# Kernel optimization log

Hardware: AMD Instinct MI355X
Metric: run time of the kernel (lower is better)

## Reference

```python
import jax, jax.numpy as jnp
import numpy as np

B, CIN, COUT, K, L = 32, 128, 128, 7, 4096
STRIDE, PAD = 1, 3
TEMP = 1.0


def setup_inputs() -> dict:
    key = jax.random.key(0)
    k1, k2 = jax.random.split(key)
    x = jax.random.normal(k1, (B, CIN, L), dtype=jnp.float32)
    weight = jax.random.normal(k2, (COUT, CIN, K), dtype=jnp.float32) * 0.1  # init: normal(0, 0.1)
    bias = jnp.zeros((COUT,), dtype=jnp.float32)
    return {"x": x, "weight": weight, "bias": bias}


def reference(x, weight, bias):
    # Soft tropical conv (intended math of the module):
    #   y[b,o,w] = T * logsumexp_{c,k}( (x[b,c,w*stride+k] + W[o,c,k]) / T ) + bias[o]
    # with -inf padding (exp(-inf)=0 => plain zero padding in exp space).
    # Computed as a numerically-stabilized standard conv in exp space, which is
    # mathematically identical and avoids materializing the (B,O,C,K,L) tensor.
    xm = jnp.max(x)
    wm = jnp.max(weight)
    ex = jnp.exp((x - xm) / TEMP)          # (B, CIN, L)
    ew = jnp.exp((weight - wm) / TEMP)     # (COUT, CIN, K)
    s = jax.lax.conv_general_dilated(
        ex, ew,
        window_strides=(STRIDE,),
        padding=[(PAD, PAD)],
        dimension_numbers=("NCH", "OIH", "NCH"),
    )  # (B, COUT, L_out); cross-correlation, matching torch unfold indexing x[i+k]
    y = TEMP * jnp.log(s) + (xm + wm)
    return y + bias[None, :, None]
```

## Files before the change

### kernel.cpp

```cpp
#include <hip/hip_runtime.h>
#include <hip/hip_bf16.h>
#include <cstdint>
#include <cstddef>

#define B_N   32
#define CIN_  128
#define COUT_ 128
#define KW_   7
#define L_    4096
#define PAD_  3
#define NW_   256
#define BC_   32
#define RPB   4104
#define NWELEM (KW_ * COUT_ * CIN_)
#define NGUARD (B_N * 8 * CIN_)

#define SW_ELEMS (KW_ * COUT_ * BC_)
#define SX_ROWS  320
#define SX_ELEMS (SX_ROWS * BC_)
#define NGRAN_W  (SW_ELEMS / 8)
#define NGRAN_T  ((SW_ELEMS + SX_ELEMS) / 8)

typedef __attribute__((ext_vector_type(8))) short  bf16x8;
typedef __attribute__((ext_vector_type(4))) float  f32x4;

__device__ __forceinline__ void gl2lds16(const void* g, void* l) {
    __builtin_amdgcn_global_load_lds(
        (const __attribute__((address_space(1))) unsigned int*)g,
        (__attribute__((address_space(3))) unsigned int*)l, 16, 0, 0);
}

__global__ __launch_bounds__(256) void exp_x_kernel(
        const float* __restrict__ x, __hip_bfloat16* __restrict__ exT,
        const float* __restrict__ w, __hip_bfloat16* __restrict__ ewb) {
    if (blockIdx.x >= 64) {
        if (blockIdx.y != 0) return;
        int base = (blockIdx.x - 64) * 256 + threadIdx.x;
        #pragma unroll
        for (int i = 0; i < 32; ++i) {
            int idx = base + 4608 * i;
            if (idx < NWELEM) {
                int c = idx & 127, rest = idx >> 7;
                int o = rest & 127, k = rest >> 7;
                ewb[idx] = __float2bfloat16(__expf(w[(o * CIN_ + c) * KW_ + k]));
            } else {
                int j  = idx - NWELEM;
                int b  = j >> 10, rr = (j >> 7) & 7, c = j & 127;
                int r  = (rr < 3) ? rr : (4096 + rr);
                exT[((size_t)b * RPB + r) * CIN_ + c] = __float2bfloat16(0.0f);
            }
        }
        return;
    }

    __shared__ __align__(16) __hip_bfloat16 tileT[64 * 136];
    const int b  = blockIdx.y;
    const int l0 = blockIdx.x * 64;
    const int tid = threadIdx.x;
    const float* xb = x + (size_t)b * CIN_ * L_ + l0;

    #pragma unroll
    for (int i = 0; i < 8; ++i) {
        int idx = tid + 256 * i;
        int c   = idx >> 4;
        int lv4 = (idx & 15) * 4;
        f32x4 v = *(const f32x4*)(xb + (size_t)c * L_ + lv4);
        #pragma unroll
        for (int k2 = 0; k2 < 4; ++k2) {
            int l  = lv4 + k2;
            int sw = (l >> 2) & 15;
            tileT[l * 136 + (c ^ (sw << 3))] = __float2bfloat16(__expf(v[k2]));
        }
    }
    __syncthreads();

    __hip_bfloat16* dst = exT + ((size_t)b * RPB + l0 + PAD_) * CIN_;
    #pragma unroll
    for (int i = 0; i < 4; ++i) {
        int idx = tid + 256 * i;
        int l  = idx >> 4;
        int gc = idx & 15;
        int sw = (l >> 2) & 15;
        bf16x8 vv = *(const bf16x8*)&tileT[l * 136 + ((gc ^ sw) << 3)];
        *(bf16x8*)(dst + (size_t)l * CIN_ + gc * 8) = vv;
    }
}

__global__ __launch_bounds__(256, 2) void tropconv_kernel(
        const __hip_bfloat16* __restrict__ exT,
        const __hip_bfloat16* __restrict__ ewb,
        const float* __restrict__ bias,
        float* __restrict__ out) {
    __shared__ __align__(16) __hip_bfloat16 smem[SW_ELEMS + SX_ELEMS];
    __hip_bfloat16* sW = smem;
    __hip_bfloat16* sX = smem + SX_ELEMS == nullptr ? nullptr : smem + SW_ELEMS;

    const int tid  = threadIdx.x;
    const int lane = tid & 63;
    const int wave = tid >> 6;
    const int wm   = wave >> 1;
    const int wn   = wave & 1;
    const int l15  = lane & 15;
    const int q    = lane >> 4;

    const int b  = blockIdx.y;
    const int w0 = blockIdx.x * NW_;
    const __hip_bfloat16* exb = exT + ((size_t)b * RPB + w0) * CIN_;

    f32x4 acc[4][8];
    #pragma unroll
    for (int i = 0; i < 4; ++i)
        #pragma unroll
        for (int j = 0; j < 8; ++j)
            acc[i][j] = (f32x4){0.f, 0.f, 0.f, 0.f};

    for (int c = 0; c < 4; ++c) {
        const int c0 = c * BC_;

        #pragma unroll
        for (int s = 0; s < 14; ++s) {
            int g  = tid + 256 * s;
            int li = g & 63;
            int blk = g >> 6;
            int t  = blk >> 3;
            int og = blk & 7;
            gl2lds16(ewb + ((((t << 7) + (og << 4) + (li & 15)) << 7) + c0 + ((li >> 4) << 3)),
                     &sW[g * 8]);
        }
        #pragma unroll
        for (int s = 0; s < 5; ++s) {
            int gx = tid + 256 * s;
            int p  = gx >> 2, j = gx & 3;
            int cj = j ^ ((p >> 1) & 3);
            gl2lds16(exb + ((size_t)p << 7) + c0 + (cj << 3), &sX[gx * 8]);
        }
        __syncthreads();

        #pragma unroll
        for (int t = 0; t < KW_; ++t) {
            bf16x8 af[4], bx[8];
            #pragma unroll
            for (int mi = 0; mi < 4; ++mi)
                af[mi] = *(const bf16x8*)&sW[((t * 8 + wm * 4 + mi) << 9) + lane * 8];
            #pragma unroll
            for (int ni = 0; ni < 8; ++ni) {
                int p = wn * 128 + ni * 16 + l15 + t;
                bx[ni] = *(const bf16x8*)&sX[(p << 5) + ((q ^ ((p >> 1) & 3)) << 3)];
            }
            #pragma unroll
            for (int mi = 0; mi < 4; ++mi)
                #pragma unroll
                for (int ni = 0; ni < 8; ++ni)
                    acc[mi][ni] = __builtin_amdgcn_mfma_f32_16x16x32_bf16(
                        af[mi], bx[ni], acc[mi][ni], 0, 0, 0);
        }
        __syncthreads();
    }

    float* outb = out + (size_t)b * COUT_ * L_;
    #pragma unroll
    for (int mi = 0; mi < 4; ++mi) {
        #pragma unroll
        for (int r = 0; r < 4; ++r) {
            int o = wm * 64 + mi * 16 + q * 4 + r;
            float bv = bias[o];
            #pragma unroll
            for (int ni = 0; ni < 8; ++ni) {
                int w = w0 + wn * 128 + ni * 16 + l15;
                outb[(size_t)o * L_ + w] = __logf(acc[mi][ni][r]) + bv;
            }
        }
    }
}

extern "C" void kernel_launch(void* const* d_in, const int* in_sizes, int n_in,
                              void* d_out, int out_size, void* d_ws, size_t ws_size,
                              hipStream_t stream) {
    const float* x    = (const float*)d_in[0];
    const float* wgt  = (const float*)d_in[1];
    const float* bias = (const float*)d_in[2];
    float* out = (float*)d_out;

    __hip_bfloat16* exT = (__hip_bfloat16*)d_ws;
    __hip_bfloat16* ewb = (__hip_bfloat16*)((char*)d_ws + (size_t)B_N * RPB * CIN_ * 2);

    exp_x_kernel<<<dim3(64 + 18, B_N), 256, 0, stream>>>(x, exT, wgt, ewb);
    tropconv_kernel<<<dim3(L_ / NW_, B_N), 256, 0, stream>>>(exT, ewb, bias, out);
}
```

Baseline: 146.8 us.

## Double-buffer LDS stages and widen tropconv block to eight waves

The channel loop is fully unrolled into a two-buffer pipeline, so the global-to-LDS loads for the next 32-channel chunk are issued while MFMAs run on the current one. The block grows to 512 threads, so each wave covers 64 rows by 64 columns instead of 128 columns and holds fewer accumulators. Staging offsets are precomputed, the X tile is trimmed to the 262 rows actually needed, and s_setprio is raised around the MFMA bursts. In exchange, LDS use roughly doubles and occupancy drops to one block per CU (launch bounds 512,1), which may limit latency hiding across blocks.

```diff
diff --git a/kernel.cpp b/kernel.cpp
--- a/kernel.cpp
+++ b/kernel.cpp
@@ -16,10 +16,8 @@
 #define NGUARD (B_N * 8 * CIN_)
 
 #define SW_ELEMS (KW_ * COUT_ * BC_)
-#define SX_ROWS  320
+#define SX_ROWS  264
 #define SX_ELEMS (SX_ROWS * BC_)
-#define NGRAN_W  (SW_ELEMS / 8)
-#define NGRAN_T  ((SW_ELEMS + SX_ELEMS) / 8)
 
 typedef __attribute__((ext_vector_type(8))) short  bf16x8;
 typedef __attribute__((ext_vector_type(4))) float  f32x4;
@@ -86,20 +84,21 @@
     }
 }
 
-__global__ __launch_bounds__(256, 2) void tropconv_kernel(
+__global__ __launch_bounds__(512, 1) void tropconv_kernel(
         const __hip_bfloat16* __restrict__ exT,
         const __hip_bfloat16* __restrict__ ewb,
         const float* __restrict__ bias,
         float* __restrict__ out) {
-    __shared__ __align__(16) __hip_bfloat16 smem[SW_ELEMS + SX_ELEMS];
-    __hip_bfloat16* sW = smem;
-    __hip_bfloat16* sX = smem + SX_ELEMS == nullptr ? nullptr : smem + SW_ELEMS;
+    __shared__ __align__(16) __hip_bfloat16 sW0[SW_ELEMS];
+    __shared__ __align__(16) __hip_bfloat16 sW1[SW_ELEMS];
+    __shared__ __align__(16) __hip_bfloat16 sX0[SX_ELEMS];
+    __shared__ __align__(16) __hip_bfloat16 sX1[SX_ELEMS];
 
     const int tid  = threadIdx.x;
     const int lane = tid & 63;
     const int wave = tid >> 6;
-    const int wm   = wave >> 1;
-    const int wn   = wave & 1;
+    const int wm   = wave >> 2;
+    const int wn   = wave & 3;
     const int l15  = lane & 15;
     const int q    = lane >> 4;
 
@@ -107,55 +106,90 @@
     const int w0 = blockIdx.x * NW_;
     const __hip_bfloat16* exb = exT + ((size_t)b * RPB + w0) * CIN_;
 
-    f32x4 acc[4][8];
+    int woff[7];
+    #pragma unroll
+    for (int s = 0; s < 7; ++s) {
+        int g  = tid + 512 * s;
+        int li = g & 63, blk = g >> 6;
+        int t  = blk >> 3, og = blk & 7;
+        woff[s] = (((t << 7) + (og << 4) + (li & 15)) << 7) + ((li >> 4) << 3);
+    }
+    int xoff[2];
+    #pragma unroll
+    for (int s = 0; s < 2; ++s) {
+        int gx = tid + 512 * s;
+        int p = gx >> 2, j = gx & 3;
+        xoff[s] = (p << 7) + (((j ^ ((p >> 1) & 3))) << 3);
+    }
+    const int gx2 = tid + 1024;
+    const int p2  = gx2 >> 2;
+    const int xoff2 = (p2 << 7) + ((((gx2 & 3) ^ ((p2 >> 1) & 3))) << 3);
+
+#define STAGE(SWB, SXB, C0)                                                  \
+    do {                                                                     \
+        _Pragma("unroll")                                                    \
+        for (int s = 0; s < 7; ++s)                                          \
+            gl2lds16(ewb + woff[s] + (C0), &SWB[(tid + 512 * s) * 8]);       \
+        _Pragma("unroll")                                                    \
+        for (int s = 0; s < 2; ++s)                                          \
+            gl2lds16(exb + xoff[s] + (C0), &SXB[(tid + 512 * s) * 8]);       \
+        if (tid < 32)                                                        \
+            gl2lds16(exb + xoff2 + (C0), &SXB[(tid + 1024) * 8]);            \
+    } while (0)
+
+#define COMPUTE(SWB, SXB)                                                    \
+    do {                                                                     \
+        _Pragma("unroll")                                                    \
+        for (int t = 0; t < KW_; ++t) {                                      \
+            bf16x8 af[4], bx[4];                                             \
+            _Pragma("unroll")                                                \
+            for (int mi = 0; mi < 4; ++mi) {                                 \
+                int blk = t * 8 + wm * 4 + mi;                               \
+                af[mi] = *(const bf16x8*)&SWB[((blk << 6) + lane) * 8];      \
+            }                                                                \
+            _Pragma("unroll")                                                \
+            for (int ni = 0; ni < 4; ++ni) {                                 \
+                int p = wn * 64 + ni * 16 + l15 + t;                         \
+                bx[ni] = *(const bf16x8*)&SXB[(p << 5) +                     \
+                                              ((q ^ ((p >> 1) & 3)) << 3)];  \
+            }                                                                \
+            __builtin_amdgcn_s_setprio(1);                                   \
+            _Pragma("unroll")                                                \
+            for (int mi = 0; mi < 4; ++mi)                                   \
+                _Pragma("unroll")                                            \
+                for (int ni = 0; ni < 4; ++ni)                               \
+                    acc[mi][ni] = __builtin_amdgcn_mfma_f32_16x16x32_bf16(   \
+                        af[mi], bx[ni], acc[mi][ni], 0, 0, 0);               \
+            __builtin_amdgcn_s_setprio(0);                                   \
+        }                                                                    \
+    } while (0)
+
+    f32x4 acc[4][4];
     #pragma unroll
     for (int i = 0; i < 4; ++i)
         #pragma unroll
-        for (int j = 0; j < 8; ++j)
+        for (int j = 0; j < 4; ++j)
             acc[i][j] = (f32x4){0.f, 0.f, 0.f, 0.f};
 
-    for (int c = 0; c < 4; ++c) {
-        const int c0 = c * BC_;
-
-        #pragma unroll
-        for (int s = 0; s < 14; ++s) {
-            int g  = tid + 256 * s;
-            int li = g & 63;
-            int blk = g >> 6;
-            int t  = blk >> 3;
-            int og = blk & 7;
-            gl2lds16(ewb + ((((t << 7) + (og << 4) + (li & 15)) << 7) + c0 + ((li >> 4) << 3)),
-                     &sW[g * 8]);
-        }
-        #pragma unroll
-        for (int s = 0; s < 5; ++s) {
-            int gx = tid + 256 * s;
-            int p  = gx >> 2, j = gx & 3;
-            int cj = j ^ ((p >> 1) & 3);
-            gl2lds16(exb + ((size_t)p << 7) + c0 + (cj << 3), &sX[gx * 8]);
-        }
-        __syncthreads();
-
-        #pragma unroll
-        for (int t = 0; t < KW_; ++t) {
-            bf16x8 af[4], bx[8];
-            #pragma unroll
-            for (int mi = 0; mi < 4; ++mi)
-                af[mi] = *(const bf16x8*)&sW[((t * 8 + wm * 4 + mi) << 9) + lane * 8];
-            #pragma unroll
-            for (int ni = 0; ni < 8; ++ni) {
-                int p = wn * 128 + ni * 16 + l15 + t;
-                bx[ni] = *(const bf16x8*)&sX[(p << 5) + ((q ^ ((p >> 1) & 3)) << 3)];
-            }
-            #pragma unroll
-            for (int mi = 0; mi < 4; ++mi)
-                #pragma unroll
-                for (int ni = 0; ni < 8; ++ni)
-                    acc[mi][ni] = __builtin_amdgcn_mfma_f32_16x16x32_bf16(
-                        af[mi], bx[ni], acc[mi][ni], 0, 0, 0);
-        }
-        __syncthreads();
-    }
+    STAGE(sW0, sX0, 0);
+    __syncthreads();
+
+    STAGE(sW1, sX1, 32);
+    COMPUTE(sW0, sX0);
+    __syncthreads();
+
+    STAGE(sW0, sX0, 64);
+    COMPUTE(sW1, sX1);
+    __syncthreads();
+
+    STAGE(sW1, sX1, 96);
+    COMPUTE(sW0, sX0);
+    __syncthreads();
+
+    COMPUTE(sW1, sX1);
+
+#undef STAGE
+#undef COMPUTE
 
     float* outb = out + (size_t)b * COUT_ * L_;
     #pragma unroll
@@ -165,8 +199,8 @@
             int o = wm * 64 + mi * 16 + q * 4 + r;
             float bv = bias[o];
             #pragma unroll
-            for (int ni = 0; ni < 8; ++ni) {
-                int w = w0 + wn * 128 + ni * 16 + l15;
+            for (int ni = 0; ni < 4; ++ni) {
+                int w = w0 + wn * 64 + ni * 16 + l15;
                 outb[(size_t)o * L_ + w] = __logf(acc[mi][ni][r]) + bv;
             }
         }
@@ -185,5 +219,5 @@
     __hip_bfloat16* ewb = (__hip_bfloat16*)((char*)d_ws + (size_t)B_N * RPB * CIN_ * 2);
 
     exp_x_kernel<<<dim3(64 + 18, B_N), 256, 0, stream>>>(x, exT, wgt, ewb);
-    tropconv_kernel<<<dim3(L_ / NW_, B_N), 256, 0, stream>>>(exT, ewb, bias, out);
-}
+    tropconv_kernel<<<dim3(L_ / NW_, B_N), 512, 0, stream>>>(exT, ewb, bias, out);
+}
```

New measurement: 148.3 us. No clear change (+1.0%).

## Stream weight fragments from global directly and stage full-channel input tile once

Applied to the files above, without the earlier changes.

The weight tensor is pre-permuted into MFMA fragment order so each wave can load A operands straight from global/L2 into registers, double-buffered across the 28 (tap, channel-chunk) steps. The input tile for all 128 channels is loaded into LDS once with an XOR swizzle, which removes the per-chunk LDS refills and barriers. MFMA bursts are wrapped in s_setprio. This trades LDS traffic and syncs for global-memory latency on weight loads and a different LDS footprint that may change occupancy.

```diff
diff --git a/kernel.cpp b/kernel.cpp
--- a/kernel.cpp
+++ b/kernel.cpp
@@ -10,16 +10,12 @@
 #define L_    4096
 #define PAD_  3
 #define NW_   256
-#define BC_   32
 #define RPB   4104
 #define NWELEM (KW_ * COUT_ * CIN_)
 #define NGUARD (B_N * 8 * CIN_)
 
-#define SW_ELEMS (KW_ * COUT_ * BC_)
-#define SX_ROWS  320
-#define SX_ELEMS (SX_ROWS * BC_)
-#define NGRAN_W  (SW_ELEMS / 8)
-#define NGRAN_T  ((SW_ELEMS + SX_ELEMS) / 8)
+#define SX_ROWS  264
+#define SX_ELEMS (SX_ROWS * CIN_)
 
 typedef __attribute__((ext_vector_type(8))) short  bf16x8;
 typedef __attribute__((ext_vector_type(4))) float  f32x4;
@@ -40,9 +36,14 @@
         for (int i = 0; i < 32; ++i) {
             int idx = base + 4608 * i;
             if (idx < NWELEM) {
-                int c = idx & 127, rest = idx >> 7;
-                int o = rest & 127, k = rest >> 7;
-                ewb[idx] = __float2bfloat16(__expf(w[(o * CIN_ + c) * KW_ + k]));
+                int e  = idx & 7;
+                int li = (idx >> 3) & 63;
+                int cc = (idx >> 9) & 3;
+                int blk = idx >> 11;
+                int og = blk & 7, t = blk >> 3;
+                int o  = og * 16 + (li & 15);
+                int ch = cc * 32 + ((li >> 4) << 3) + e;
+                ewb[idx] = __float2bfloat16(__expf(w[(o * CIN_ + ch) * KW_ + t]));
             } else {
                 int j  = idx - NWELEM;
                 int b  = j >> 10, rr = (j >> 7) & 7, c = j & 127;
@@ -91,9 +92,7 @@
         const __hip_bfloat16* __restrict__ ewb,
         const float* __restrict__ bias,
         float* __restrict__ out) {
-    __shared__ __align__(16) __hip_bfloat16 smem[SW_ELEMS + SX_ELEMS];
-    __hip_bfloat16* sW = smem;
-    __hip_bfloat16* sX = smem + SX_ELEMS == nullptr ? nullptr : smem + SW_ELEMS;
+    __shared__ __align__(16) __hip_bfloat16 sX[SX_ELEMS];
 
     const int tid  = threadIdx.x;
     const int lane = tid & 63;
@@ -107,6 +106,18 @@
     const int w0 = blockIdx.x * NW_;
     const __hip_bfloat16* exb = exT + ((size_t)b * RPB + w0) * CIN_;
 
+    #pragma unroll
+    for (int s = 0; s < 16; ++s) {
+        int gx = tid + 256 * s;
+        int p = gx >> 4, j = gx & 15;
+        gl2lds16(exb + (p << 7) + ((j ^ (p & 7)) << 3), &sX[gx * 8]);
+    }
+    if (tid < 128) {
+        int gx = tid + 4096;
+        int p = gx >> 4, j = gx & 15;
+        gl2lds16(exb + (p << 7) + ((j ^ (p & 7)) << 3), &sX[gx * 8]);
+    }
+
     f32x4 acc[4][8];
     #pragma unroll
     for (int i = 0; i < 4; ++i)
@@ -114,48 +125,69 @@
         for (int j = 0; j < 8; ++j)
             acc[i][j] = (f32x4){0.f, 0.f, 0.f, 0.f};
 
-    for (int c = 0; c < 4; ++c) {
-        const int c0 = c * BC_;
-
-        #pragma unroll
-        for (int s = 0; s < 14; ++s) {
-            int g  = tid + 256 * s;
-            int li = g & 63;
-            int blk = g >> 6;
-            int t  = blk >> 3;
-            int og = blk & 7;
-            gl2lds16(ewb + ((((t << 7) + (og << 4) + (li & 15)) << 7) + c0 + ((li >> 4) << 3)),
-                     &sW[g * 8]);
-        }
-        #pragma unroll
-        for (int s = 0; s < 5; ++s) {
-            int gx = tid + 256 * s;
-            int p  = gx >> 2, j = gx & 3;
-            int cj = j ^ ((p >> 1) & 3);
-            gl2lds16(exb + ((size_t)p << 7) + c0 + (cj << 3), &sX[gx * 8]);
-        }
-        __syncthreads();
-
-        #pragma unroll
-        for (int t = 0; t < KW_; ++t) {
-            bf16x8 af[4], bx[8];
-            #pragma unroll
-            for (int mi = 0; mi < 4; ++mi)
-                af[mi] = *(const bf16x8*)&sW[((t * 8 + wm * 4 + mi) << 9) + lane * 8];
-            #pragma unroll
-            for (int ni = 0; ni < 8; ++ni) {
-                int p = wn * 128 + ni * 16 + l15 + t;
-                bx[ni] = *(const bf16x8*)&sX[(p << 5) + ((q ^ ((p >> 1) & 3)) << 3)];
-            }
-            #pragma unroll
-            for (int mi = 0; mi < 4; ++mi)
-                #pragma unroll
-                for (int ni = 0; ni < 8; ++ni)
-                    acc[mi][ni] = __builtin_amdgcn_mfma_f32_16x16x32_bf16(
-                        af[mi], bx[ni], acc[mi][ni], 0, 0, 0);
-        }
-        __syncthreads();
-    }
+    __syncthreads();
+
+#define ALOAD(AF, T, CC)                                                     \
+    do {                                                                     \
+        _Pragma("unroll")                                                    \
+        for (int mi = 0; mi < 4; ++mi)                                       \
+            AF[mi] = *(const bf16x8*)&ewb[(((((T) * 8 + wm * 4 + mi) * 4     \
+                                             + (CC)) << 6) + lane) * 8];     \
+    } while (0)
+
+#define BDOT(AF, T, CC)                                                      \
+    do {                                                                     \
+        bf16x8 bx[8];                                                        \
+        _Pragma("unroll")                                                    \
+        for (int ni = 0; ni < 8; ++ni) {                                     \
+            int p = wn * 128 + ni * 16 + l15 + (T);                          \
+            int g = ((CC) * 4 + q) ^ (p & 7);                                \
+            bx[ni] = *(const bf16x8*)&sX[(p << 7) + (g << 3)];               \
+        }                                                                    \
+        __builtin_amdgcn_s_setprio(1);                                       \
+        _Pragma("unroll")                                                    \
+        for (int mi = 0; mi < 4; ++mi)                                       \
+            _Pragma("unroll")                                                \
+            for (int ni = 0; ni < 8; ++ni)                                   \
+                acc[mi][ni] = __builtin_amdgcn_mfma_f32_16x16x32_bf16(       \
+                    AF[mi], bx[ni], acc[mi][ni], 0, 0, 0);                   \
+        __builtin_amdgcn_s_setprio(0);                                       \
+    } while (0)
+
+    {
+        bf16x8 afA[4], afB[4];
+        ALOAD(afA, 0, 0);
+        ALOAD(afB, 1, 0);  BDOT(afA, 0, 0);
+        ALOAD(afA, 2, 0);  BDOT(afB, 1, 0);
+        ALOAD(afB, 3, 0);  BDOT(afA, 2, 0);
+        ALOAD(afA, 4, 0);  BDOT(afB, 3, 0);
+        ALOAD(afB, 5, 0);  BDOT(afA, 4, 0);
+        ALOAD(afA, 6, 0);  BDOT(afB, 5, 0);
+        ALOAD(afB, 0, 1);  BDOT(afA, 6, 0);
+        ALOAD(afA, 1, 1);  BDOT(afB, 0, 1);
+        ALOAD(afB, 2, 1);  BDOT(afA, 1, 1);
+        ALOAD(afA, 3, 1);  BDOT(afB, 2, 1);
+        ALOAD(afB, 4, 1);  BDOT(afA, 3, 1);
+        ALOAD(afA, 5, 1);  BDOT(afB, 4, 1);
+        ALOAD(afB, 6, 1);  BDOT(afA, 5, 1);
+        ALOAD(afA, 0, 2);  BDOT(afB, 6, 1);
+        ALOAD(afB, 1, 2);  BDOT(afA, 0, 2);
+        ALOAD(afA, 2, 2);  BDOT(afB, 1, 2);
+        ALOAD(afB, 3, 2);  BDOT(afA, 2, 2);
+        ALOAD(afA, 4, 2);  BDOT(afB, 3, 2);
+        ALOAD(afB, 5, 2);  BDOT(afA, 4, 2);
+        ALOAD(afA, 6, 2);  BDOT(afB, 5, 2);
+        ALOAD(afB, 0, 3);  BDOT(afA, 6, 2);
+        ALOAD(afA, 1, 3);  BDOT(afB, 0, 3);
+        ALOAD(afB, 2, 3);  BDOT(afA, 1, 3);
+        ALOAD(afA, 3, 3);  BDOT(afB, 2, 3);
+        ALOAD(afB, 4, 3);  BDOT(afA, 3, 3);
+        ALOAD(afA, 5, 3);  BDOT(afB, 4, 3);
+        ALOAD(afB, 6, 3);  BDOT(afA, 5, 3);
+                           BDOT(afB, 6, 3);
+    }
+#undef ALOAD
+#undef BDOT
 
     float* outb = out + (size_t)b * COUT_ * L_;
     #pragma unroll
```

New measurement: 143.9 us. 1.02x faster.

## Stage full-channel input tile once, stream weights from global, use 32x32 MFMA

Applied to the files above, without the earlier changes.

The conv kernel now loads the whole 264-row by 128-channel input tile into LDS once, instead of in four channel chunks with barriers, and drops weight staging in LDS. Weights are pre-permuted into a fragment-friendly layout by the exp kernel and read directly from global/L2 into registers with a 3-deep software prefetch. The MFMA is switched from 16x16x32 to 32x32x16 bf16. This removes the per-chunk syncs and LDS weight traffic and raises the MFMA work per operand read. In exchange it depends on global weight-load latency being hidden by the prefetch, and the larger LDS tile may change occupancy.

```diff
diff --git a/kernel.cpp b/kernel.cpp
--- a/kernel.cpp
+++ b/kernel.cpp
@@ -10,19 +10,16 @@
 #define L_    4096
 #define PAD_  3
 #define NW_   256
-#define BC_   32
 #define RPB   4104
 #define NWELEM (KW_ * COUT_ * CIN_)
 #define NGUARD (B_N * 8 * CIN_)
 
-#define SW_ELEMS (KW_ * COUT_ * BC_)
-#define SX_ROWS  320
-#define SX_ELEMS (SX_ROWS * BC_)
-#define NGRAN_W  (SW_ELEMS / 8)
-#define NGRAN_T  ((SW_ELEMS + SX_ELEMS) / 8)
+#define SX_ROWS  264
+#define SX_ELEMS (SX_ROWS * CIN_)
 
-typedef __attribute__((ext_vector_type(8))) short  bf16x8;
-typedef __attribute__((ext_vector_type(4))) float  f32x4;
+typedef __attribute__((ext_vector_type(8)))  short bf16x8;
+typedef __attribute__((ext_vector_type(4)))  float f32x4;
+typedef __attribute__((ext_vector_type(16))) float f32x16;
 
 __device__ __forceinline__ void gl2lds16(const void* g, void* l) {
     __builtin_amdgcn_global_load_lds(
@@ -40,9 +37,15 @@
         for (int i = 0; i < 32; ++i) {
             int idx = base + 4608 * i;
             if (idx < NWELEM) {
-                int c = idx & 127, rest = idx >> 7;
-                int o = rest & 127, k = rest >> 7;
-                ewb[idx] = __float2bfloat16(__expf(w[(o * CIN_ + c) * KW_ + k]));
+                int e   = idx & 7;
+                int l6  = (idx >> 3) & 63;
+                int frg = idx >> 9;
+                int oq  = frg & 3;
+                int ck  = (frg >> 2) & 7;
+                int t   = frg >> 5;
+                int o   = oq * 32 + (l6 & 31);
+                int ch  = ck * 16 + ((l6 >> 5) << 3) + e;
+                ewb[idx] = __float2bfloat16(__expf(w[(o * CIN_ + ch) * KW_ + t]));
             } else {
                 int j  = idx - NWELEM;
                 int b  = j >> 10, rr = (j >> 7) & 7, c = j & 127;
@@ -91,82 +94,88 @@
         const __hip_bfloat16* __restrict__ ewb,
         const float* __restrict__ bias,
         float* __restrict__ out) {
-    __shared__ __align__(16) __hip_bfloat16 smem[SW_ELEMS + SX_ELEMS];
-    __hip_bfloat16* sW = smem;
-    __hip_bfloat16* sX = smem + SX_ELEMS == nullptr ? nullptr : smem + SW_ELEMS;
+    __shared__ __align__(16) __hip_bfloat16 sX[SX_ELEMS];
 
     const int tid  = threadIdx.x;
     const int lane = tid & 63;
     const int wave = tid >> 6;
     const int wm   = wave >> 1;
     const int wn   = wave & 1;
-    const int l15  = lane & 15;
-    const int q    = lane >> 4;
+    const int l31  = lane & 31;
+    const int h    = lane >> 5;
 
     const int b  = blockIdx.y;
     const int w0 = blockIdx.x * NW_;
     const __hip_bfloat16* exb = exT + ((size_t)b * RPB + w0) * CIN_;
 
-    f32x4 acc[4][8];
     #pragma unroll
-    for (int i = 0; i < 4; ++i)
+    for (int s = 0; s < 16; ++s) {
+        int gx = tid + 256 * s;
+        int p = gx >> 4, j = gx & 15;
+        gl2lds16(exb + (p << 7) + ((j ^ (p & 15)) << 3), &sX[gx * 8]);
+    }
+    if (tid < 128) {
+        int gx = tid + 4096;
+        int p = gx >> 4, j = gx & 15;
+        gl2lds16(exb + (p << 7) + ((j ^ (p & 15)) << 3), &sX[gx * 8]);
+    }
+
+    f32x16 acc[2][4];
+    #pragma unroll
+    for (int i = 0; i < 2; ++i)
         #pragma unroll
-        for (int j = 0; j < 8; ++j)
-            acc[i][j] = (f32x4){0.f, 0.f, 0.f, 0.f};
+        for (int j = 0; j < 4; ++j)
+            #pragma unroll
+            for (int r = 0; r < 16; ++r)
+                acc[i][j][r] = 0.f;
 
-    for (int c = 0; c < 4; ++c) {
-        const int c0 = c * BC_;
+    bf16x8 afq[4][2];
+#define ALOADP(P)                                                            \
+    do {                                                                     \
+        if ((P) < 56) {                                                      \
+            _Pragma("unroll")                                                \
+            for (int mi = 0; mi < 2; ++mi)                                   \
+                afq[(P) & 3][mi] = *(const bf16x8*)&ewb[                     \
+                    (((((P) % 7) * 8 + (P) / 7) * 4 + wm * 2 + mi) << 9)     \
+                    + lane * 8];                                             \
+        }                                                                    \
+    } while (0)
 
+    ALOADP(0); ALOADP(1); ALOADP(2);
+
+    __syncthreads();
+
+    #pragma unroll
+    for (int ph = 0; ph < 56; ++ph) {
+        ALOADP(ph + 3);
+        const int t_  = ph % 7;
+        const int ck_ = ph / 7;
+        bf16x8 bx[4];
         #pragma unroll
-        for (int s = 0; s < 14; ++s) {
-            int g  = tid + 256 * s;
-            int li = g & 63;
-            int blk = g >> 6;
-            int t  = blk >> 3;
-            int og = blk & 7;
-            gl2lds16(ewb + ((((t << 7) + (og << 4) + (li & 15)) << 7) + c0 + ((li >> 4) << 3)),
-                     &sW[g * 8]);
+        for (int ni = 0; ni < 4; ++ni) {
+            int p = wn * 128 + ni * 32 + l31 + t_;
+            int s = (ck_ * 2 + h) ^ (p & 15);
+            bx[ni] = *(const bf16x8*)&sX[(p << 7) + (s << 3)];
         }
         #pragma unroll
-        for (int s = 0; s < 5; ++s) {
-            int gx = tid + 256 * s;
-            int p  = gx >> 2, j = gx & 3;
-            int cj = j ^ ((p >> 1) & 3);
-            gl2lds16(exb + ((size_t)p << 7) + c0 + (cj << 3), &sX[gx * 8]);
-        }
-        __syncthreads();
-
-        #pragma unroll
-        for (int t = 0; t < KW_; ++t) {
-            bf16x8 af[4], bx[8];
+        for (int mi = 0; mi < 2; ++mi)
             #pragma unroll
-            for (int mi = 0; mi < 4; ++mi)
-                af[mi] = *(const bf16x8*)&sW[((t * 8 + wm * 4 + mi) << 9) + lane * 8];
-            #pragma unroll
-            for (int ni = 0; ni < 8; ++ni) {
-                int p = wn * 128 + ni * 16 + l15 + t;
-                bx[ni] = *(const bf16x8*)&sX[(p << 5) + ((q ^ ((p >> 1) & 3)) << 3)];
-            }
-            #pragma unroll
-            for (int mi = 0; mi < 4; ++mi)
-                #pragma unroll
-                for (int ni = 0; ni < 8; ++ni)
-                    acc[mi][ni] = __builtin_amdgcn_mfma_f32_16x16x32_bf16(
-                        af[mi], bx[ni], acc[mi][ni], 0, 0, 0);
-        }
-        __syncthreads();
+            for (int ni = 0; ni < 4; ++ni)
+                acc[mi][ni] = __builtin_amdgcn_mfma_f32_32x32x16_bf16(
+                    afq[ph & 3][mi], bx[ni], acc[mi][ni], 0, 0, 0);
     }
+#undef ALOADP
 
     float* outb = out + (size_t)b * COUT_ * L_;
     #pragma unroll
-    for (int mi = 0; mi < 4; ++mi) {
+    for (int mi = 0; mi < 2; ++mi) {
         #pragma unroll
-        for (int r = 0; r < 4; ++r) {
-            int o = wm * 64 + mi * 16 + q * 4 + r;
+        for (int r = 0; r < 16; ++r) {
+            int o = (wm * 2 + mi) * 32 + (r & 3) + 8 * (r >> 2) + 4 * h;
             float bv = bias[o];
             #pragma unroll
-            for (int ni = 0; ni < 8; ++ni) {
-                int w = w0 + wn * 128 + ni * 16 + l15;
+            for (int ni = 0; ni < 4; ++ni) {
+                int w = w0 + wn * 128 + ni * 32 + l31;
                 outb[(size_t)o * L_ + w] = __logf(acc[mi][ni][r]) + bv;
             }
         }
```

New measurement: 157.5 us. 1.07x slower.
